# Performance work log

Hardware: AMD Instinct MI355X
Metric: run time of the kernel (lower is better)

## Reference

```python
import jax, jax.numpy as jnp
import numpy as np

HEADS = 16
DIM_HEAD = 64
MAX_REL_POS = 1024   # temporal_length
TEXT_LEN = 77
IMG_SCALE = 1.0      # image_cross_attention_scale


def setup_inputs() -> dict:
    key = jax.random.key(0)
    ks = jax.random.split(key, 12)
    B, N, D = 32, 1024, 1024
    CTX = TEXT_LEN + 256
    s = 0.02
    return {
        "x": jax.random.normal(ks[0], (B, N, D), jnp.float32),
        "context": jax.random.normal(ks[1], (B, CTX, D), jnp.float32),
        "W_q": jax.random.normal(ks[2], (D, D), jnp.float32) * s,
        "W_k": jax.random.normal(ks[3], (D, D), jnp.float32) * s,
        "W_v": jax.random.normal(ks[4], (D, D), jnp.float32) * s,
        "W_k_ip": jax.random.normal(ks[5], (D, D), jnp.float32) * s,
        "W_v_ip": jax.random.normal(ks[6], (D, D), jnp.float32) * s,
        "rel_k": jax.random.normal(ks[7], (2 * MAX_REL_POS + 1, DIM_HEAD), jnp.float32) * s,
        "rel_v": jax.random.normal(ks[8], (2 * MAX_REL_POS + 1, DIM_HEAD), jnp.float32) * s,
        "W_out": jax.random.normal(ks[9], (D, D), jnp.float32) * s,
        "b_out": jnp.zeros((D,), jnp.float32),
        "alpha": jnp.zeros((1,), jnp.float32),
    }


def _split_heads(t):
    # [b, n, h*d] -> [b, h, n, d]
    b, n, _ = t.shape
    return t.reshape(b, n, HEADS, DIM_HEAD).transpose(0, 2, 1, 3)


def _merge_heads(t):
    # [b, h, n, d] -> [b, n, h*d]
    b, h, n, d = t.shape
    return t.transpose(0, 2, 1, 3).reshape(b, n, h * d)


def _rel_embeddings(table, len_q, len_k):
    # gather relative-position embeddings: [len_q, len_k, d]
    dist = jnp.arange(len_k)[None, :] - jnp.arange(len_q)[:, None]
    idx = jnp.clip(dist, -MAX_REL_POS, MAX_REL_POS) + MAX_REL_POS
    return table[idx]


def reference(x, context, W_q, W_k, W_v, W_k_ip, W_v_ip, rel_k, rel_v, W_out, b_out, alpha):
    scale = DIM_HEAD ** -0.5
    ctx_text = context[:, :TEXT_LEN, :]
    ctx_img = context[:, TEXT_LEN:, :]

    q = _split_heads(x @ W_q)          # [b,h,i,d]
    k = _split_heads(ctx_text @ W_k)   # [b,h,j,d]
    v = _split_heads(ctx_text @ W_v)

    sim = jnp.einsum('bhid,bhjd->bhij', q, k) * scale
    len_q, len_k = q.shape[2], k.shape[2]
    k2 = _rel_embeddings(rel_k, len_q, len_k)            # [i,j,d]
    sim = sim + jnp.einsum('bhid,ijd->bhij', q, k2) * scale
    attn = jax.nn.softmax(sim, axis=-1)

    out = jnp.einsum('bhij,bhjd->bhid', attn, v)
    v2 = _rel_embeddings(rel_v, len_q, len_k)            # [i,j,d]
    out = out + jnp.einsum('bhij,ijd->bhid', attn, v2)
    out = _merge_heads(out)                              # [b,i,h*d]

    # second image-context KV stream
    k_ip = _split_heads(ctx_img @ W_k_ip)
    v_ip = _split_heads(ctx_img @ W_v_ip)
    sim_ip = jnp.einsum('bhid,bhjd->bhij', q, k_ip) * scale
    attn_ip = jax.nn.softmax(sim_ip, axis=-1)
    out_ip = _merge_heads(jnp.einsum('bhij,bhjd->bhid', attn_ip, v_ip))

    # learnable-scale bypass: out + scale * out_ip * (tanh(alpha)+1)
    out = out + IMG_SCALE * out_ip * (jnp.tanh(alpha[0]) + 1.0)
    return out @ W_out + b_out
```

## Files before the change

kernel.cpp:

```cpp
#include <hip/hip_runtime.h>
#include <math.h>

typedef __bf16 bf16_t;
typedef __bf16 bf16x2 __attribute__((ext_vector_type(2)));
typedef __bf16 bf16x8 __attribute__((ext_vector_type(8)));
typedef float f32x4 __attribute__((ext_vector_type(4)));

#define BATCH   32
#define SEQ     1024
#define DMODEL  1024
#define NHEADS  16
#define DIMH    64
#define TEXTLEN 77
#define IMGLEN  256
#define CTXLEN  333
#define MAXREL  1024

#define MFMA16(a,b,c) __builtin_amdgcn_mfma_f32_16x16x32_bf16(a, b, c, 0, 0, 0)
#define SCALE_LOG2E 0.1803368809f

__device__ __forceinline__ unsigned pk2(float a, float b) {
  union { bf16x2 v; unsigned u; } t;
  t.v[0] = (bf16_t)a; t.v[1] = (bf16_t)b;
  return t.u;
}

__global__ __launch_bounds__(256) void k_cvt_x(const float* __restrict__ in,
                                               bf16_t* __restrict__ out) {
  size_t idx = ((size_t)blockIdx.x * blockDim.x + threadIdx.x) * 8;
  float4 a = *(const float4*)(in + idx);
  float4 b = *(const float4*)(in + idx + 4);
  bf16x8 o;
  o[0] = (bf16_t)a.x; o[1] = (bf16_t)a.y; o[2] = (bf16_t)a.z; o[3] = (bf16_t)a.w;
  o[4] = (bf16_t)b.x; o[5] = (bf16_t)b.y; o[6] = (bf16_t)b.z; o[7] = (bf16_t)b.w;
  *(bf16x8*)(out + idx) = o;
}

__global__ __launch_bounds__(128) void k_cvt_ctx(const float* __restrict__ ctx,
                                                 bf16_t* __restrict__ ctxT,
                                                 bf16_t* __restrict__ ctxI) {
  int row = blockIdx.x;
  int b = row / CTXLEN, t = row - b * CTXLEN;
  const float* src = ctx + (size_t)row * DMODEL + threadIdx.x * 8;
  bf16_t* dst = (t < TEXTLEN)
      ? ctxT + ((size_t)(b * 80 + t)) * DMODEL + threadIdx.x * 8
      : ctxI + ((size_t)(b * IMGLEN + (t - TEXTLEN))) * DMODEL + threadIdx.x * 8;
  float4 a = *(const float4*)(src);
  float4 c = *(const float4*)(src + 4);
  bf16x8 o;
  o[0] = (bf16_t)a.x; o[1] = (bf16_t)a.y; o[2] = (bf16_t)a.z; o[3] = (bf16_t)a.w;
  o[4] = (bf16_t)c.x; o[5] = (bf16_t)c.y; o[6] = (bf16_t)c.z; o[7] = (bf16_t)c.w;
  *(bf16x8*)dst = o;
  if (t == 0) {
    bf16x8 z = {};
    #pragma unroll
    for (int rr = 77; rr < 80; ++rr)
      *(bf16x8*)(ctxT + ((size_t)(b * 80 + rr)) * DMODEL + threadIdx.x * 8) = z;
  }
}

__global__ void k_transpose_w(const float* __restrict__ W, bf16_t* __restrict__ WT) {
  __shared__ float tile[32][33];
  int x = threadIdx.x, y = threadIdx.y;
  int n0 = blockIdx.x * 32, k0 = blockIdx.y * 32;
  #pragma unroll
  for (int r = 0; r < 32; r += 8)
    tile[y + r][x] = W[(size_t)(k0 + y + r) * DMODEL + n0 + x];
  __syncthreads();
  #pragma unroll
  for (int r = 0; r < 32; r += 8)
    WT[(size_t)(n0 + y + r) * DMODEL + k0 + x] = (bf16_t)tile[x][y + r];
}

__global__ __launch_bounds__(256) void k_cvt_relk(const float* __restrict__ relk,
                                                  bf16_t* __restrict__ Rkb) {
  int idx = blockIdx.x * 256 + threadIdx.x;
  int u = idx >> 3, d0 = (idx & 7) * 8;
  const float* s = relk + (size_t)(u + 1) * DIMH + d0;
  float4 a = *(const float4*)s;
  float4 b = *(const float4*)(s + 4);
  bf16x8 o;
  o[0] = (bf16_t)a.x; o[1] = (bf16_t)a.y; o[2] = (bf16_t)a.z; o[3] = (bf16_t)a.w;
  o[4] = (bf16_t)b.x; o[5] = (bf16_t)b.y; o[6] = (bf16_t)b.z; o[7] = (bf16_t)b.w;
  *(bf16x8*)(Rkb + (size_t)u * DIMH + d0) = o;
}

__global__ __launch_bounds__(256) void k_cvt_relvT(const float* __restrict__ relv,
                                                   bf16_t* __restrict__ RvT) {
  int idx = blockIdx.x * 256 + threadIdx.x;
  int d = idx >> 8, u0 = (idx & 255) * 8;
  bf16x8 o;
  #pragma unroll
  for (int e = 0; e < 8; ++e)
    o[e] = (bf16_t)relv[(size_t)(u0 + e + 1) * DIMH + d];
  *(bf16x8*)(RvT + (size_t)d * 2048 + u0) = o;
}

typedef __attribute__((address_space(1))) void gvoid;
typedef __attribute__((address_space(3))) void svoid;

__device__ __forceinline__ void async_ld16(const void* g, void* l) {
  __builtin_amdgcn_global_load_lds((gvoid*)g, (svoid*)l, 16, 0, 0);
}

template<int STORE, bool AHM>
__global__ __launch_bounds__(512) void k_gemm(
    const bf16_t* __restrict__ A16, const bf16_t* __restrict__ BT,
    void* __restrict__ Cout, void* __restrict__ Cout2,
    const float* __restrict__ bias, int M, int N, int K)
{
  __shared__ __align__(16) bf16_t lds_a[2][256 * 32];
  __shared__ __align__(16) bf16_t lds_b[2][128 * 32];
  const int tid = threadIdx.x;
  const int wid = tid >> 6, lane = tid & 63;
  const int nx = gridDim.x, ny = gridDim.y;
  const int lin = blockIdx.y * nx + blockIdx.x;
  const int nwg = nx * ny;
  const int swz = (lin & 7) * (nwg >> 3) + (lin >> 3);
  const int bcol = (swz % ny) * 128;
  const int brow = (swz / ny) * 256;
  const int wr = (wid >> 1) * 64, wc = (wid & 1) * 64;
  const int lhi = lane >> 4, llo = lane & 15;

  auto stage = [&](int kk, int buf) __attribute__((always_inline)) {
    #pragma unroll
    for (int ch = 0; ch < 2; ++ch) {
      int cid = ch * 512 + tid;
      int row = cid >> 2, ccol = cid & 3;
      int gcol = (ccol ^ (row & 3)) << 3;
      const bf16_t* src;
      if constexpr (AHM) {
        int grow = brow + row;
        src = A16 + (((size_t)((grow >> 10) * 16 + (kk >> 6)) * 1024 + (grow & 1023)) << 6)
              + (kk & 32) + gcol;
      } else {
        src = A16 + (size_t)(brow + row) * K + kk + gcol;
      }
      async_ld16(src, (char*)lds_a[buf] + cid * 16);
    }
    {
      int row = tid >> 2, ccol = tid & 3;
      int gcol = (ccol ^ (row & 3)) << 3;
      async_ld16(BT + (size_t)(bcol + row) * K + kk + gcol,
                 (char*)lds_b[buf] + tid * 16);
    }
  };

  f32x4 acc[4][4];
  #pragma unroll
  for (int m = 0; m < 4; ++m)
    #pragma unroll
    for (int n = 0; n < 4; ++n)
      acc[m][n] = (f32x4){0.f, 0.f, 0.f, 0.f};

  stage(0, 0);
  int cur = 0;
  for (int kk = 0; kk < K; kk += 32) {
    if (kk + 32 < K) {
      stage(kk + 32, cur ^ 1);
      __builtin_amdgcn_sched_barrier(0);
      asm volatile("s_waitcnt vmcnt(3)" ::: "memory");
      __builtin_amdgcn_sched_barrier(0);
    } else {
      asm volatile("s_waitcnt vmcnt(0)" ::: "memory");
    }
    __builtin_amdgcn_s_barrier();

    bf16x8 af[4], bfv[4];
    #pragma unroll
    for (int m = 0; m < 4; ++m) {
      int row = wr + m * 16 + llo;
      af[m] = *(const bf16x8*)((const char*)lds_a[cur] + row * 64
                               + ((lhi ^ (row & 3)) << 4));
    }
    #pragma unroll
    for (int n = 0; n < 4; ++n) {
      int row = wc + n * 16 + llo;
      bfv[n] = *(const bf16x8*)((const char*)lds_b[cur] + row * 64
                                + ((lhi ^ (row & 3)) << 4));
    }
    #pragma unroll
    for (int m = 0; m < 4; ++m)
      #pragma unroll
      for (int n = 0; n < 4; ++n)
        acc[m][n] = MFMA16(af[m], bfv[n], acc[m][n]);

    asm volatile("s_waitcnt lgkmcnt(0)" ::: "memory");
    __builtin_amdgcn_sched_barrier(0);
    __builtin_amdgcn_s_barrier();
    cur ^= 1;
  }

  #pragma unroll
  for (int m = 0; m < 4; ++m)
    #pragma unroll
    for (int n = 0; n < 4; ++n) {
      const int gc = bcol + wc + n * 16 + llo;
      #pragma unroll
      for (int r = 0; r < 4; ++r) {
        const int gr = brow + wr + m * 16 + lhi * 4 + r;
        float v = acc[m][n][r];
        if constexpr (STORE == 2) {
          ((float*)Cout)[(size_t)gr * N + gc] = v + bias[gc];
        } else if constexpr (STORE == 4) {
          int hh2 = gc >> 6;
          ((bf16_t*)Cout)[((((size_t)((gr >> 10) * 16 + hh2)) << 10) + (gr & 1023)) * 64
                          + (gc & 63)] = (bf16_t)v;
        } else if constexpr (STORE == 5) {
          int bb = (gr * 6554) >> 19;
          int jj = gr - bb * 80;
          int hh2 = (gc & 1023) >> 6;
          bf16_t* dst = (gc < 1024) ? (bf16_t*)Cout : (bf16_t*)Cout2;
          dst[(((size_t)(bb * 16 + hh2) * 80 + jj) << 6) + (gc & 63)] = (bf16_t)v;
        } else {
          int bb = gr >> 8, uu = gr & 255;
          int hh2 = (gc & 1023) >> 6;
          bf16_t* dst = (gc < 1024) ? (bf16_t*)Cout : (bf16_t*)Cout2;
          dst[((((size_t)(bb * 16 + hh2)) << 8) + uu) * 64 + (gc & 63)] = (bf16_t)v;
        }
      }
    }
}

template<int RPB, int OUTC>
__global__ __launch_bounds__(256) void k_vtrans(const bf16_t* __restrict__ V,
                                                bf16_t* __restrict__ Vt) {
  __shared__ bf16_t tile[64][72];
  const int nt = (OUTC + 63) / 64;
  const int u0 = (blockIdx.x % nt) * 64;
  const int bh = blockIdx.x / nt;
  const int tid = threadIdx.x;
  const int ur = tid >> 2, cg = (tid & 3) * 16;
  {
    const bf16_t* src = V + (((size_t)bh * RPB + u0 + ur) << 6) + cg;
    *(bf16x8*)&tile[ur][cg] = *(const bf16x8*)src;
    *(bf16x8*)&tile[ur][cg + 8] = *(const bf16x8*)(src + 8);
  }
  __syncthreads();
  bf16x8 o0, o1;
  #pragma unroll
  for (int e = 0; e < 8; ++e) { o0[e] = tile[cg + e][ur]; o1[e] = tile[cg + 8 + e][ur]; }
  bf16_t* dst = Vt + (size_t)bh * 64 * OUTC + (size_t)ur * OUTC + u0 + cg;
  if (u0 + cg + 8 <= OUTC)  *(bf16x8*)dst = o0;
  if (u0 + cg + 16 <= OUTC) *(bf16x8*)(dst + 8) = o1;
}

__global__ __launch_bounds__(256, 3) void k_txt(
    const bf16_t* __restrict__ Qh,
    const bf16_t* __restrict__ Kth,
    const bf16_t* __restrict__ Vtt,
    const bf16_t* __restrict__ Rkb,
    const bf16_t* __restrict__ RvT,
    bf16_t* __restrict__ Oh)
{
  __shared__ __align__(16) bf16_t kt_l[80 * 64];
  __shared__ __align__(16) char p_l[4][6400];
  __shared__ __align__(16) char olds[4][2048];
  const int tid = threadIdx.x;
  const int w = tid >> 6, lane = tid & 63;
  const int c = lane & 15, g = lane >> 4;
  const int bh = blockIdx.x;

  #pragma unroll
  for (int q = 0; q < 3; ++q) {
    int cid0 = q * 256 + w * 64;
    if (cid0 < 640) {
      int cid = cid0 + lane;
      int row = cid >> 3, cc = cid & 7;
      const bf16_t* src = Kth + (((size_t)bh * 80 + row) << 6) + ((cc ^ (row & 7)) << 3);
      async_ld16(src, (char*)kt_l + cid0 * 16);
    }
  }
  __syncthreads();

  bf16_t* p = (bf16_t*)p_l[w];
  const bf16_t* qbase = Qh + ((size_t)bh << 16);
  const bf16_t* vbase = Vtt + (size_t)bh * 5120;

  bf16x8 qa0, qa1;
  {
    const bf16_t* qp = qbase + ((size_t)(w * 256 + c) << 6) + g * 8;
    qa0 = *(const bf16x8*)qp;
    qa1 = *(const bf16x8*)(qp + 32);
  }

  for (int st = 0; st < 16; ++st) {
    const int iq = w * 256 + st * 16;
    const int ub = 1008 - iq;
    bf16x8 qn0 = qa0, qn1 = qa1;
    if (st < 15) {
      const bf16_t* qp = qbase + ((size_t)(iq + 16 + c) << 6) + g * 8;
      qn0 = *(const bf16x8*)qp;
      qn1 = *(const bf16x8*)(qp + 32);
    }
    f32x4 ta[6];
    #pragma unroll
    for (int n = 0; n < 6; ++n) ta[n] = (f32x4){0.f, 0.f, 0.f, 0.f};
    {
      const bf16_t* rp = Rkb + (size_t)(ub + c) * DIMH + g * 8;
      #pragma unroll
      for (int n = 0; n < 6; ++n) {
        bf16x8 b0 = *(const bf16x8*)(rp + n * 16 * DIMH);
        bf16x8 b1 = *(const bf16x8*)(rp + n * 16 * DIMH + 32);
        ta[n] = MFMA16(qa0, b0, ta[n]);
        ta[n] = MFMA16(qa1, b1, ta[n]);
      }
    }
    f32x4 s[5];
    #pragma unroll
    for (int n = 0; n < 5; ++n) s[n] = (f32x4){0.f, 0.f, 0.f, 0.f};
    {
      const int sw = (c & 7) << 4;
      #pragma unroll
      for (int n = 0; n < 5; ++n) {
        int rb = (n * 16 + c) * 128;
        bf16x8 k0 = *(const bf16x8*)((const char*)kt_l + rb + ((g << 4) ^ sw));
        bf16x8 k1 = *(const bf16x8*)((const char*)kt_l + rb + (((4 + g) << 4) ^ sw));
        s[n] = MFMA16(qa0, k0, s[n]);
        s[n] = MFMA16(qa1, k1, s[n]);
      }
    }
    float st4[5][4];
    #pragma unroll
    for (int r = 0; r < 4; ++r) {
      int il = 4 * g + r;
      int cz = c + 15 - il;
      int srcl = (lane & 48) | (cz & 15);
      bool lo_pick = (cz >> 4) == 0;
      #pragma unroll
      for (int n = 0; n < 5; ++n) {
        float tlo = __shfl(ta[n][r], srcl);
        float thi = __shfl(ta[n + 1][r], srcl);
        float tv = lo_pick ? tlo : thi;
        int j = 16 * n + c;
        st4[n][r] = (j < TEXTLEN) ? (s[n][r] + tv) : -1e30f;
      }
    }
    float rsum[4];
    #pragma unroll
    for (int r = 0; r < 4; ++r) {
      float m = st4[0][r];
      #pragma unroll
      for (int n = 1; n < 5; ++n) m = fmaxf(m, st4[n][r]);
      m = fmaxf(m, __shfl_xor(m, 1));
      m = fmaxf(m, __shfl_xor(m, 2));
      m = fmaxf(m, __shfl_xor(m, 4));
      m = fmaxf(m, __shfl_xor(m, 8));
      float ssum = 0.f;
      #pragma unroll
      for (int n = 0; n < 5; ++n) {
        float pv = exp2f((st4[n][r] - m) * SCALE_LOG2E);
        st4[n][r] = pv;
        ssum += pv;
      }
      ssum += __shfl_xor(ssum, 1);
      ssum += __shfl_xor(ssum, 2);
      ssum += __shfl_xor(ssum, 4);
      ssum += __shfl_xor(ssum, 8);
      rsum[r] = ssum;
    }
    {
      bf16x8 z8 = {};
      #pragma unroll
      for (int z = 0; z < 7; ++z) {
        int off = z * 1024 + lane * 16;
        if (off < 6400)
          *(bf16x8*)((char*)p + off) = z8;
      }
      #pragma unroll
      for (int n = 0; n < 5; ++n)
        #pragma unroll
        for (int r = 0; r < 4; ++r) {
          int j = 16 * n + c;
          if (j < TEXTLEN) {
            int il = 4 * g + r;
            bf16_t pb = (bf16_t)st4[n][r];
            p[il * 200 + (j + 15 - il)] = pb;
            p[il * 200 + 96 + j] = pb;
          }
        }
    }
    f32x4 ot[4];
    #pragma unroll
    for (int dt = 0; dt < 4; ++dt) ot[dt] = (f32x4){0.f, 0.f, 0.f, 0.f};
    #pragma unroll
    for (int kt = 0; kt < 6; ++kt) {
      bf16x8 pf = *(const bf16x8*)(p + c * 200 + kt * 32 + g * 8);
      int klo = kt * 32 + g * 8;
      #pragma unroll
      for (int dt = 0; dt < 4; ++dt) {
        int d = dt * 16 + c;
        bf16x8 af;
        if (klo < 96) {
          af = *(const bf16x8*)(RvT + (size_t)d * 2048 + ub + klo);
        } else {
          int uv = klo - 96;
          uv = (uv > 72) ? 72 : uv;
          af = *(const bf16x8*)(vbase + d * 80 + uv);
        }
        ot[dt] = MFMA16(af, pf, ot[dt]);
      }
    }
    int srcq = ((c >> 2) << 4) | c;
    float t0 = __shfl(rsum[0], srcq);
    float t1 = __shfl(rsum[1], srcq);
    float t2 = __shfl(rsum[2], srcq);
    float t3 = __shfl(rsum[3], srcq);
    float rs = (c & 2) ? ((c & 1) ? t3 : t2) : ((c & 1) ? t1 : t0);
    float inv = 1.f / rs;
    #pragma unroll
    for (int dt = 0; dt < 4; ++dt) {
      int chunk = dt * 2 + (g >> 1);
      char* pa = olds[w] + c * 128 + ((chunk ^ (c & 7)) << 4) + (g & 1) * 8;
      uint2 nv;
      nv.x = pk2(ot[dt][0] * inv, ot[dt][1] * inv);
      nv.y = pk2(ot[dt][2] * inv, ot[dt][3] * inv);
      *(uint2*)pa = nv;
    }
    char* ob = (char*)(Oh + (((size_t)bh * 1024 + iq) << 6));
    #pragma unroll
    for (int k2 = 0; k2 < 2; ++k2) {
      int k = k2 * 64 + lane, rr = k >> 3, cc = k & 7;
      uint4 v = *(uint4*)(olds[w] + rr * 128 + ((cc ^ (rr & 7)) << 4));
      *(uint4*)(ob + rr * 128 + cc * 16) = v;
    }
    qa0 = qn0; qa1 = qn1;
  }
}

__global__ __launch_bounds__(256, 2) void k_img(
    const bf16_t* __restrict__ Qh,
    const bf16_t* __restrict__ Khi,
    const bf16_t* __restrict__ Vipt,
    const float* __restrict__ alpha,
    bf16_t* __restrict__ Oh)
{
  __shared__ __align__(16) bf16_t kst[256 * 64];
  __shared__ __align__(16) bf16_t vst[64 * 256];
  __shared__ __align__(16) char olds[4][2048];
  const int tid = threadIdx.x;
  const int w = tid >> 6, lane = tid & 63;
  const int c = lane & 15, g = lane >> 4;
  const int i0 = blockIdx.x * 512;
  const int bh = blockIdx.y;

  #pragma unroll
  for (int q = 0; q < 8; ++q) {
    int cid = q * 256 + tid;
    int row = cid >> 3, cc = cid & 7;
    const bf16_t* src = Khi + (((size_t)bh * 256 + row) << 6) + ((cc ^ (row & 7)) << 3);
    async_ld16(src, (char*)kst + q * 4096 + w * 1024);
  }
  const char* vsrc0 = (const char*)(Vipt + (size_t)bh * 16384);
  #pragma unroll
  for (int q = 0; q < 8; ++q) {
    int L = (q * 256 + tid) * 16;
    int row = L >> 9;
    async_ld16(vsrc0 + (L ^ ((row & 7) << 4)), (char*)vst + q * 4096 + w * 1024);
  }
  {
    int iq = i0 + w * 128;
    #pragma unroll
    for (int k2 = 0; k2 < 2; ++k2) {
      int k = k2 * 64 + lane, rr = k >> 3, cc = k & 7;
      async_ld16(Oh + (((size_t)bh * 1024 + iq + rr) << 6) + ((cc ^ (rr & 7)) << 3),
                 olds[w] + k2 * 1024);
    }
  }
  __syncthreads();

  const float coef = tanhf(alpha[0]) + 1.0f;
  const bf16_t* qbase = Qh + ((size_t)bh << 16);

  bf16x8 qa0, qa1;
  {
    const bf16_t* qp = qbase + ((size_t)(i0 + w * 128 + c) << 6) + g * 8;
    qa0 = *(const bf16x8*)qp;
    qa1 = *(const bf16x8*)(qp + 32);
  }

  for (int st = 0; st < 8; ++st) {
    const int iq = i0 + w * 128 + st * 16;
    bf16x8 qn0 = qa0, qn1 = qa1;
    if (st < 7) {
      const bf16_t* qp = qbase + ((size_t)(iq + 16 + c) << 6) + g * 8;
      qn0 = *(const bf16x8*)qp;
      qn1 = *(const bf16x8*)(qp + 32);
    }
    f32x4 acc[4];
    #pragma unroll
    for (int dt = 0; dt < 4; ++dt) acc[dt] = (f32x4){0.f, 0.f, 0.f, 0.f};
    float m_run = -1e30f, l_run = 0.f;

    #pragma unroll
    for (int jt = 0; jt < 2; ++jt) {
      f32x4 s2[8];
      #pragma unroll
      for (int n = 0; n < 8; ++n) s2[n] = (f32x4){0.f, 0.f, 0.f, 0.f};
      const int sw = (c & 7) << 4;
      #pragma unroll
      for (int n = 0; n < 8; ++n) {
        int rb = (jt * 128 + n * 16 + c) * 128;
        bf16x8 k0 = *(const bf16x8*)((const char*)kst + rb + ((g << 4) ^ sw));
        bf16x8 k1 = *(const bf16x8*)((const char*)kst + rb + (((4 + g) << 4) ^ sw));
        s2[n] = MFMA16(k0, qa0, s2[n]);
        s2[n] = MFMA16(k1, qa1, s2[n]);
      }
      float mx = -1e30f;
      #pragma unroll
      for (int n = 0; n < 8; ++n)
        #pragma unroll
        for (int r = 0; r < 4; ++r) mx = fmaxf(mx, s2[n][r]);
      mx = fmaxf(mx, __shfl_xor(mx, 16));
      mx = fmaxf(mx, __shfl_xor(mx, 32));
      float m_new = fmaxf(m_run, mx);
      float fscale = exp2f((m_run - m_new) * SCALE_LOG2E);
      float tsum = 0.f;
      #pragma unroll
      for (int n = 0; n < 8; ++n)
        #pragma unroll
        for (int r = 0; r < 4; ++r) {
          float pv = exp2f((s2[n][r] - m_new) * SCALE_LOG2E);
          s2[n][r] = pv; tsum += pv;
        }
      tsum += __shfl_xor(tsum, 16);
      tsum += __shfl_xor(tsum, 32);
      l_run = l_run * fscale + tsum;
      m_run = m_new;
      #pragma unroll
      for (int dt = 0; dt < 4; ++dt) acc[dt] *= fscale;
      const int srcA = c | ((g & 1) << 5);
      const int srcB = srcA + 16;
      const bool hi_n = ((g >> 1) & 1) != 0;
      #pragma unroll
      for (int kt = 0; kt < 4; ++kt) {
        unsigned lo0 = pk2(s2[2 * kt][0], s2[2 * kt][1]);
        unsigned hi0 = pk2(s2[2 * kt][2], s2[2 * kt][3]);
        unsigned lo1 = pk2(s2[2 * kt + 1][0], s2[2 * kt + 1][1]);
        unsigned hi1 = pk2(s2[2 * kt + 1][2], s2[2 * kt + 1][3]);
        unsigned a0 = __shfl(lo0, srcA), a1 = __shfl(lo1, srcA);
        unsigned b0 = __shfl(hi0, srcA), b1 = __shfl(hi1, srcA);
        unsigned c0 = __shfl(lo0, srcB), c1 = __shfl(lo1, srcB);
        unsigned d0 = __shfl(hi0, srcB), d1 = __shfl(hi1, srcB);
        union { unsigned u[4]; bf16x8 v; } pf;
        pf.u[0] = hi_n ? a1 : a0;
        pf.u[1] = hi_n ? b1 : b0;
        pf.u[2] = hi_n ? c1 : c0;
        pf.u[3] = hi_n ? d1 : d0;
        #pragma unroll
        for (int dt = 0; dt < 4; ++dt) {
          int d = dt * 16 + c;
          int a = (d * 512 + jt * 256 + kt * 64 + g * 16) ^ ((c & 7) << 4);
          bf16x8 vf = *(const bf16x8*)((const char*)vst + a);
          acc[dt] = MFMA16(vf, pf.v, acc[dt]);
        }
      }
    }
    float inv = coef / l_run;
    asm volatile("s_waitcnt vmcnt(0)" ::: "memory");
    #pragma unroll
    for (int dt = 0; dt < 4; ++dt) {
      int chunk = dt * 2 + (g >> 1);
      char* pa = olds[w] + c * 128 + ((chunk ^ (c & 7)) << 4) + (g & 1) * 8;
      union { uint2 u2; bf16_t e[4]; } ov; ov.u2 = *(uint2*)pa;
      uint2 nv;
      nv.x = pk2((float)ov.e[0] + acc[dt][0] * inv, (float)ov.e[1] + acc[dt][1] * inv);
      nv.y = pk2((float)ov.e[2] + acc[dt][2] * inv, (float)ov.e[3] + acc[dt][3] * inv);
      *(uint2*)pa = nv;
    }
    char* ob = (char*)(Oh + (((size_t)bh * 1024 + iq) << 6));
    #pragma unroll
    for (int k2 = 0; k2 < 2; ++k2) {
      int k = k2 * 64 + lane, rr = k >> 3, cc = k & 7;
      uint4 v = *(uint4*)(olds[w] + rr * 128 + ((cc ^ (rr & 7)) << 4));
      *(uint4*)(ob + rr * 128 + cc * 16) = v;
    }
    asm volatile("s_waitcnt lgkmcnt(0)" ::: "memory");
    if (st < 7) {
      int iqn = iq + 16;
      #pragma unroll
      for (int k2 = 0; k2 < 2; ++k2) {
        int k = k2 * 64 + lane, rr = k >> 3, cc = k & 7;
        async_ld16(Oh + (((size_t)bh * 1024 + iqn + rr) << 6) + ((cc ^ (rr & 7)) << 3),
                   olds[w] + k2 * 1024);
      }
    }
    qa0 = qn0; qa1 = qn1;
  }
}

extern "C" void kernel_launch(void* const* d_in, const int* in_sizes, int n_in,
                              void* d_out, int out_size, void* d_ws, size_t ws_size,
                              hipStream_t stream)
{
  const float* x     = (const float*)d_in[0];
  const float* ctx   = (const float*)d_in[1];
  const float* W_q   = (const float*)d_in[2];
  const float* W_k   = (const float*)d_in[3];
  const float* W_v   = (const float*)d_in[4];
  const float* W_kip = (const float*)d_in[5];
  const float* W_vip = (const float*)d_in[6];
  const float* rel_k = (const float*)d_in[7];
  const float* rel_v = (const float*)d_in[8];
  const float* W_out = (const float*)d_in[9];
  const float* b_out = (const float*)d_in[10];
  const float* alpha = (const float*)d_in[11];

  char* ws = (char*)d_ws;
  bf16_t* Oh   = (bf16_t*)(ws + 0);
  bf16_t* Qh   = (bf16_t*)(ws + 67108864);
  bf16_t* CtxT = (bf16_t*)(ws + 134217728);
  bf16_t* CtxI = (bf16_t*)(ws + 139460608);
  bf16_t* WTs  = (bf16_t*)(ws + 156237824);
  bf16_t* WqT   = WTs + 0 * 1048576;
  bf16_t* WkT   = WTs + 1 * 1048576;
  bf16_t* WvT   = WTs + 2 * 1048576;
  bf16_t* WkipT = WTs + 3 * 1048576;
  bf16_t* WvipT = WTs + 4 * 1048576;
  bf16_t* WoutT = WTs + 5 * 1048576;

  char* dob = (char*)d_out;
  bf16_t* Khi   = (bf16_t*)(dob + 0);
  bf16_t* Vhi   = (bf16_t*)(dob + 16777216);
  bf16_t* Vipt  = (bf16_t*)(dob + 33554432);
  bf16_t* Kth   = (bf16_t*)(dob + 50331648);
  bf16_t* Vth   = (bf16_t*)(dob + 55574528);
  bf16_t* Vtt   = (bf16_t*)(dob + 60817408);
  bf16_t* Rkb   = (bf16_t*)(dob + 66060288);
  bf16_t* RvT   = (bf16_t*)(dob + 66322432);
  bf16_t* Xb    = (bf16_t*)(dob + 66584576);

  k_cvt_x<<<16384, 256, 0, stream>>>(x, Xb);
  k_cvt_ctx<<<BATCH * CTXLEN, 128, 0, stream>>>(ctx, CtxT, CtxI);
  dim3 tb(32, 8), tg(32, 32);
  k_transpose_w<<<tg, tb, 0, stream>>>(W_q,   WqT);
  k_transpose_w<<<tg, tb, 0, stream>>>(W_k,   WkT);
  k_transpose_w<<<tg, tb, 0, stream>>>(W_v,   WvT);
  k_transpose_w<<<tg, tb, 0, stream>>>(W_kip, WkipT);
  k_transpose_w<<<tg, tb, 0, stream>>>(W_vip, WvipT);
  k_transpose_w<<<tg, tb, 0, stream>>>(W_out, WoutT);
  k_cvt_relk<<<64, 256, 0, stream>>>(rel_k, Rkb);
  k_cvt_relvT<<<64, 256, 0, stream>>>(rel_v, RvT);

  k_gemm<4, false><<<dim3(128, 8),  512, 0, stream>>>(Xb,   WqT,   (void*)Qh,  nullptr,     nullptr, 32768, 1024, 1024);
  k_gemm<5, false><<<dim3(10, 16),  512, 0, stream>>>(CtxT, WkT,   (void*)Kth, (void*)Vth,  nullptr, 2560,  2048, 1024);
  k_gemm<6, false><<<dim3(32, 16),  512, 0, stream>>>(CtxI, WkipT, (void*)Khi, (void*)Vhi,  nullptr, 8192,  2048, 1024);

  k_vtrans<80,  80 ><<<2 * 512, 256, 0, stream>>>(Vth, Vtt);
  k_vtrans<256, 256><<<4 * 512, 256, 0, stream>>>(Vhi, Vipt);

  k_txt<<<512, 256, 0, stream>>>(Qh, Kth, Vtt, Rkb, RvT, Oh);
  k_img<<<dim3(2, 512), 256, 0, stream>>>(Qh, Khi, Vipt, alpha, Oh);

  k_gemm<2, true><<<dim3(128, 8), 512, 0, stream>>>(Oh, WoutT, d_out, nullptr, b_out, 32768, 1024, 1024);
}
```

Baseline: 579.8 us.

## Split text-attention grid over query halves and stage V in shared memory

The text-attention kernel now launches two blocks per batch-head, each covering half of the queries, which doubles the block count. The V tile is preloaded into LDS with a rotated swizzle instead of being read from global memory. The single combined P staging buffer is split into two smaller passes (relative-V, then V), which shrinks per-wave LDS. This is meant to raise parallelism and occupancy and to cut global V loads. In exchange the K and V tiles are loaded twice per batch-head and each step has an extra zero-fill pass.

```diff
diff --git a/kernel.cpp b/kernel.cpp
--- a/kernel.cpp
+++ b/kernel.cpp
@@ -254,12 +254,14 @@
     bf16_t* __restrict__ Oh)
 {
   __shared__ __align__(16) bf16_t kt_l[80 * 64];
-  __shared__ __align__(16) char p_l[4][6400];
+  __shared__ __align__(16) bf16_t vt_l[64 * 80];
+  __shared__ __align__(16) char p_l[4][3328];
   __shared__ __align__(16) char olds[4][2048];
   const int tid = threadIdx.x;
   const int w = tid >> 6, lane = tid & 63;
   const int c = lane & 15, g = lane >> 4;
-  const int bh = blockIdx.x;
+  const int half = blockIdx.x;
+  const int bh = blockIdx.y;
 
   #pragma unroll
   for (int q = 0; q < 3; ++q) {
@@ -271,24 +273,35 @@
       async_ld16(src, (char*)kt_l + cid0 * 16);
     }
   }
+  #pragma unroll
+  for (int q = 0; q < 3; ++q) {
+    int cid0 = q * 256 + w * 64;
+    if (cid0 < 640) {
+      int cid = cid0 + lane;
+      int row = cid / 10;
+      int col = cid - row * 10;
+      int colp = col - (row & 7); if (colp < 0) colp += 10;
+      const bf16_t* src = Vtt + (size_t)bh * 5120 + row * 80 + colp * 8;
+      async_ld16(src, (char*)vt_l + cid0 * 16);
+    }
+  }
   __syncthreads();
 
   bf16_t* p = (bf16_t*)p_l[w];
   const bf16_t* qbase = Qh + ((size_t)bh << 16);
-  const bf16_t* vbase = Vtt + (size_t)bh * 5120;
 
   bf16x8 qa0, qa1;
   {
-    const bf16_t* qp = qbase + ((size_t)(w * 256 + c) << 6) + g * 8;
+    const bf16_t* qp = qbase + ((size_t)(half * 512 + w * 128 + c) << 6) + g * 8;
     qa0 = *(const bf16x8*)qp;
     qa1 = *(const bf16x8*)(qp + 32);
   }
 
-  for (int st = 0; st < 16; ++st) {
-    const int iq = w * 256 + st * 16;
+  for (int st = 0; st < 8; ++st) {
+    const int iq = half * 512 + w * 128 + st * 16;
     const int ub = 1008 - iq;
     bf16x8 qn0 = qa0, qn1 = qa1;
-    if (st < 15) {
+    if (st < 7) {
       const bf16_t* qp = qbase + ((size_t)(iq + 16 + c) << 6) + g * 8;
       qn0 = *(const bf16x8*)qp;
       qn1 = *(const bf16x8*)(qp + 32);
@@ -359,13 +372,15 @@
       ssum += __shfl_xor(ssum, 8);
       rsum[r] = ssum;
     }
+    f32x4 ot[4];
+    #pragma unroll
+    for (int dt = 0; dt < 4; ++dt) ot[dt] = (f32x4){0.f, 0.f, 0.f, 0.f};
     {
       bf16x8 z8 = {};
       #pragma unroll
-      for (int z = 0; z < 7; ++z) {
+      for (int z = 0; z < 4; ++z) {
         int off = z * 1024 + lane * 16;
-        if (off < 6400)
-          *(bf16x8*)((char*)p + off) = z8;
+        if (off < 3328) *(bf16x8*)((char*)p + off) = z8;
       }
       #pragma unroll
       for (int n = 0; n < 5; ++n)
@@ -374,31 +389,50 @@
           int j = 16 * n + c;
           if (j < TEXTLEN) {
             int il = 4 * g + r;
-            bf16_t pb = (bf16_t)st4[n][r];
-            p[il * 200 + (j + 15 - il)] = pb;
-            p[il * 200 + 96 + j] = pb;
+            p[il * 104 + (j + 15 - il)] = (bf16_t)st4[n][r];
           }
         }
-    }
-    f32x4 ot[4];
-    #pragma unroll
-    for (int dt = 0; dt < 4; ++dt) ot[dt] = (f32x4){0.f, 0.f, 0.f, 0.f};
-    #pragma unroll
-    for (int kt = 0; kt < 6; ++kt) {
-      bf16x8 pf = *(const bf16x8*)(p + c * 200 + kt * 32 + g * 8);
-      int klo = kt * 32 + g * 8;
-      #pragma unroll
-      for (int dt = 0; dt < 4; ++dt) {
-        int d = dt * 16 + c;
-        bf16x8 af;
-        if (klo < 96) {
-          af = *(const bf16x8*)(RvT + (size_t)d * 2048 + ub + klo);
-        } else {
-          int uv = klo - 96;
-          uv = (uv > 72) ? 72 : uv;
-          af = *(const bf16x8*)(vbase + d * 80 + uv);
+      #pragma unroll
+      for (int kt = 0; kt < 3; ++kt) {
+        bf16x8 pf = *(const bf16x8*)(p + c * 104 + kt * 32 + g * 8);
+        int klo = kt * 32 + g * 8;
+        #pragma unroll
+        for (int dt = 0; dt < 4; ++dt) {
+          int d = dt * 16 + c;
+          bf16x8 af = *(const bf16x8*)(RvT + (size_t)d * 2048 + ub + klo);
+          ot[dt] = MFMA16(af, pf, ot[dt]);
         }
-        ot[dt] = MFMA16(af, pf, ot[dt]);
+      }
+    }
+    {
+      bf16x8 z8 = {};
+      #pragma unroll
+      for (int z = 0; z < 4; ++z) {
+        int off = z * 1024 + lane * 16;
+        if (off < 3328) *(bf16x8*)((char*)p + off) = z8;
+      }
+      #pragma unroll
+      for (int n = 0; n < 5; ++n)
+        #pragma unroll
+        for (int r = 0; r < 4; ++r) {
+          int j = 16 * n + c;
+          if (j < TEXTLEN) {
+            int il = 4 * g + r;
+            p[il * 104 + j] = (bf16_t)st4[n][r];
+          }
+        }
+      #pragma unroll
+      for (int kt = 0; kt < 3; ++kt) {
+        bf16x8 pf = *(const bf16x8*)(p + c * 104 + kt * 32 + g * 8);
+        int klo = kt * 32 + g * 8;
+        #pragma unroll
+        for (int dt = 0; dt < 4; ++dt) {
+          int d = dt * 16 + c;
+          int chunk = (klo >> 3) + (c & 7);
+          if (chunk >= 10) chunk -= 10;
+          bf16x8 af = *(const bf16x8*)((const char*)vt_l + d * 160 + chunk * 16);
+          ot[dt] = MFMA16(af, pf, ot[dt]);
+        }
       }
     }
     int srcq = ((c >> 2) << 4) | c;
@@ -649,7 +683,7 @@
   k_vtrans<80,  80 ><<<2 * 512, 256, 0, stream>>>(Vth, Vtt);
   k_vtrans<256, 256><<<4 * 512, 256, 0, stream>>>(Vhi, Vipt);
 
-  k_txt<<<512, 256, 0, stream>>>(Qh, Kth, Vtt, Rkb, RvT, Oh);
+  k_txt<<<dim3(2, 512), 256, 0, stream>>>(Qh, Kth, Vtt, Rkb, RvT, Oh);
   k_img<<<dim3(2, 512), 256, 0, stream>>>(Qh, Khi, Vipt, alpha, Oh);
 
   k_gemm<2, true><<<dim3(128, 8), 512, 0, stream>>>(Oh, WoutT, d_out, nullptr, b_out, 32768, 1024, 1024);
```

New measurement: 608.8 us. 5.0% more time.

## Split text attention across two query halves and stage V in LDS

Applied to the files above, without the earlier changes.

The text-attention kernel now launches two blocks per (batch, head), each covering half the queries, which doubles the grid from 512 to 1024 blocks to fill more CUs. The text V tile is loaded into shared memory once per block with a rotated-chunk swizzle, replacing per-lane global reads. The six weight-transpose launches are merged into one launch with a z dimension. In exchange, K/V are loaded twice per head, the extra LDS may lower occupancy, and the swizzle arithmetic must match the old clamped indexing.

```diff
diff --git a/kernel.cpp b/kernel.cpp
--- a/kernel.cpp
+++ b/kernel.cpp
@@ -59,8 +59,14 @@
   }
 }
 
-__global__ void k_transpose_w(const float* __restrict__ W, bf16_t* __restrict__ WT) {
+__global__ void k_transpose_w6(const float* __restrict__ W0, const float* __restrict__ W1,
+                               const float* __restrict__ W2, const float* __restrict__ W3,
+                               const float* __restrict__ W4, const float* __restrict__ W5,
+                               bf16_t* __restrict__ WTs) {
   __shared__ float tile[32][33];
+  const float* Ws[6] = {W0, W1, W2, W3, W4, W5};
+  const float* W = Ws[blockIdx.z];
+  bf16_t* WT = WTs + (size_t)blockIdx.z * 1048576;
   int x = threadIdx.x, y = threadIdx.y;
   int n0 = blockIdx.x * 32, k0 = blockIdx.y * 32;
   #pragma unroll
@@ -254,12 +260,14 @@
     bf16_t* __restrict__ Oh)
 {
   __shared__ __align__(16) bf16_t kt_l[80 * 64];
+  __shared__ __align__(16) bf16_t vt_l[64 * 80];
   __shared__ __align__(16) char p_l[4][6400];
   __shared__ __align__(16) char olds[4][2048];
   const int tid = threadIdx.x;
   const int w = tid >> 6, lane = tid & 63;
   const int c = lane & 15, g = lane >> 4;
-  const int bh = blockIdx.x;
+  const int half = blockIdx.x;
+  const int bh = blockIdx.y;
 
   #pragma unroll
   for (int q = 0; q < 3; ++q) {
@@ -271,24 +279,35 @@
       async_ld16(src, (char*)kt_l + cid0 * 16);
     }
   }
+  #pragma unroll
+  for (int q = 0; q < 3; ++q) {
+    int cid0 = q * 256 + w * 64;
+    if (cid0 < 640) {
+      int cid = cid0 + lane;
+      int row = cid / 10;
+      int col = cid - row * 10;
+      int colp = col - (row & 7); if (colp < 0) colp += 10;
+      const bf16_t* src = Vtt + (size_t)bh * 5120 + row * 80 + colp * 8;
+      async_ld16(src, (char*)vt_l + cid0 * 16);
+    }
+  }
   __syncthreads();
 
   bf16_t* p = (bf16_t*)p_l[w];
   const bf16_t* qbase = Qh + ((size_t)bh << 16);
-  const bf16_t* vbase = Vtt + (size_t)bh * 5120;
 
   bf16x8 qa0, qa1;
   {
-    const bf16_t* qp = qbase + ((size_t)(w * 256 + c) << 6) + g * 8;
+    const bf16_t* qp = qbase + ((size_t)(half * 512 + w * 128 + c) << 6) + g * 8;
     qa0 = *(const bf16x8*)qp;
     qa1 = *(const bf16x8*)(qp + 32);
   }
 
-  for (int st = 0; st < 16; ++st) {
-    const int iq = w * 256 + st * 16;
+  for (int st = 0; st < 8; ++st) {
+    const int iq = half * 512 + w * 128 + st * 16;
     const int ub = 1008 - iq;
     bf16x8 qn0 = qa0, qn1 = qa1;
-    if (st < 15) {
+    if (st < 7) {
       const bf16_t* qp = qbase + ((size_t)(iq + 16 + c) << 6) + g * 8;
       qn0 = *(const bf16x8*)qp;
       qn1 = *(const bf16x8*)(qp + 32);
@@ -395,8 +414,8 @@
           af = *(const bf16x8*)(RvT + (size_t)d * 2048 + ub + klo);
         } else {
           int uv = klo - 96;
-          uv = (uv > 72) ? 72 : uv;
-          af = *(const bf16x8*)(vbase + d * 80 + uv);
+          int chunk = (uv >> 3) + (c & 7); if (chunk >= 10) chunk -= 10;
+          af = *(const bf16x8*)((const char*)vt_l + d * 160 + chunk * 16);
         }
         ot[dt] = MFMA16(af, pf, ot[dt]);
       }
@@ -614,9 +633,7 @@
   bf16_t* WTs  = (bf16_t*)(ws + 156237824);
   bf16_t* WqT   = WTs + 0 * 1048576;
   bf16_t* WkT   = WTs + 1 * 1048576;
-  bf16_t* WvT   = WTs + 2 * 1048576;
   bf16_t* WkipT = WTs + 3 * 1048576;
-  bf16_t* WvipT = WTs + 4 * 1048576;
   bf16_t* WoutT = WTs + 5 * 1048576;
 
   char* dob = (char*)d_out;
@@ -632,13 +649,7 @@
 
   k_cvt_x<<<16384, 256, 0, stream>>>(x, Xb);
   k_cvt_ctx<<<BATCH * CTXLEN, 128, 0, stream>>>(ctx, CtxT, CtxI);
-  dim3 tb(32, 8), tg(32, 32);
-  k_transpose_w<<<tg, tb, 0, stream>>>(W_q,   WqT);
-  k_transpose_w<<<tg, tb, 0, stream>>>(W_k,   WkT);
-  k_transpose_w<<<tg, tb, 0, stream>>>(W_v,   WvT);
-  k_transpose_w<<<tg, tb, 0, stream>>>(W_kip, WkipT);
-  k_transpose_w<<<tg, tb, 0, stream>>>(W_vip, WvipT);
-  k_transpose_w<<<tg, tb, 0, stream>>>(W_out, WoutT);
+  k_transpose_w6<<<dim3(32, 32, 6), dim3(32, 8), 0, stream>>>(W_q, W_k, W_v, W_kip, W_vip, W_out, WTs);
   k_cvt_relk<<<64, 256, 0, stream>>>(rel_k, Rkb);
   k_cvt_relvT<<<64, 256, 0, stream>>>(rel_v, RvT);
 
@@ -649,7 +660,7 @@
   k_vtrans<80,  80 ><<<2 * 512, 256, 0, stream>>>(Vth, Vtt);
   k_vtrans<256, 256><<<4 * 512, 256, 0, stream>>>(Vhi, Vipt);
 
-  k_txt<<<512, 256, 0, stream>>>(Qh, Kth, Vtt, Rkb, RvT, Oh);
+  k_txt<<<dim3(2, 512), 256, 0, stream>>>(Qh, Kth, Vtt, Rkb, RvT, Oh);
   k_img<<<dim3(2, 512), 256, 0, stream>>>(Qh, Khi, Vipt, alpha, Oh);
 
   k_gemm<2, true><<<dim3(128, 8), 512, 0, stream>>>(Oh, WoutT, d_out, nullptr, b_out, 32768, 1024, 1024);
```

After: 558.2 us. 3.7% less time.
